# Performance work log

Hardware: AMD Instinct MI355X
Metric: run time of the kernel (lower is better)

Reference implementation:

```python
import jax, jax.numpy as jnp
import numpy as np

B, C, CE, DK, DV, H, W = 2, 64, 96, 64, 64, 96, 96
EPS = 1e-6


def setup_inputs() -> dict:
    key = jax.random.key(0)
    ks = jax.random.split(key, 8)
    s = lambda fan_in: 1.0 / np.sqrt(fan_in)
    return {
        "x": jax.random.normal(ks[0], (B, C, H, W), jnp.float32),
        "x_enc": jax.random.normal(ks[1], (B, CE, H, W), jnp.float32),
        "Wq": jax.random.uniform(ks[2], (DK, CE), jnp.float32, -s(CE), s(CE)),
        "bq": jax.random.uniform(ks[3], (DK,), jnp.float32, -s(CE), s(CE)),
        "Wk": jax.random.uniform(ks[4], (DK, CE), jnp.float32, -s(CE), s(CE)),
        "bk": jax.random.uniform(ks[5], (DK,), jnp.float32, -s(CE), s(CE)),
        "Wv": jax.random.uniform(ks[6], (DV, C), jnp.float32, -s(C), s(C)),
        "bv": jax.random.uniform(ks[7], (DV,), jnp.float32, -s(C), s(C)),
    }


def _l2norm(t):
    # F.normalize(dim=1): divide by channel-dim L2 norm, clamped at eps
    n = jnp.maximum(jnp.linalg.norm(t, axis=1, keepdims=True), EPS)
    return t / n


def reference(x, x_enc, Wq, bq, Wk, bk, Wv, bv):
    # 1x1 conv projections == pointwise channel GEMMs
    Q = jnp.einsum('oc,bchw->bohw', Wq, x_enc) + bq[None, :, None, None]
    K = jnp.einsum('oc,bchw->bohw', Wk, x_enc) + bk[None, :, None, None]
    V = jnp.einsum('oc,bchw->bohw', Wv, x) + bv[None, :, None, None]
    vshape = V.shape
    Q = _l2norm(Q.reshape(B, DK, H * W))  # [B, dk, L]
    K = _l2norm(K.reshape(B, DK, H * W))
    V = V.reshape(B, DV, H * W)           # [B, dv, L]
    # cosine-similarity attention over all spatial positions: A is [B, L, L]
    A = jax.nn.softmax(jnp.einsum('bqi,bqj->bij', Q, K), axis=-1)
    R = jnp.einsum('bij,bvj->bvi', A, V)   # [B, dv, L]
    return R.reshape(vshape)
```

## Files before the change

kernel.cpp:

```cpp
#include <hip/hip_runtime.h>

#define L_ 9216

typedef unsigned int uint;
typedef unsigned short ushort;
typedef __attribute__((ext_vector_type(8))) short short8;
typedef __attribute__((ext_vector_type(4))) float f32x4;
typedef __attribute__((ext_vector_type(16))) float f32x16;
typedef __attribute__((ext_vector_type(4))) unsigned uint4v;
typedef __attribute__((ext_vector_type(2))) unsigned uint2v;

#define MFMA32(a, b, c) __builtin_amdgcn_mfma_f32_32x32x16_bf16(a, b, c, 0, 0, 0)

#if __has_builtin(__builtin_amdgcn_exp2f)
#define EXP2(x) __builtin_amdgcn_exp2f(x)
#else
#define EXP2(x) exp2f(x)
#endif

#define GLOAD_LDS16(g, l)                                            \
  __builtin_amdgcn_global_load_lds(                                  \
      (const __attribute__((address_space(1))) unsigned int*)(g),    \
      (__attribute__((address_space(3))) unsigned int*)(l), 16, 0, 0)

union B8 {
  uint4v u;
  short8 s;
};

__device__ __forceinline__ ushort f2bf(float f) {
  uint u = __float_as_uint(f);
  return (ushort)((u + 0x7fffu + ((u >> 16) & 1u)) >> 16);
}

__device__ __forceinline__ f32x16 zero16() {
  f32x16 v;
#pragma unroll
  for (int i = 0; i < 16; i++) v[i] = 0.f;
  return v;
}

__global__ __launch_bounds__(256) void prep_kernel(
    const float* __restrict__ Wq, const float* __restrict__ Wk,
    const float* __restrict__ Wv, ushort* __restrict__ Wqb,
    ushort* __restrict__ Wkb, ushort* __restrict__ Wvb) {
  int i = blockIdx.x * 256 + threadIdx.x;
  if (i < 6144) {
    Wqb[i] = f2bf(Wq[i]);
    Wkb[i] = f2bf(Wk[i]);
  }
  if (i < 4096) Wvb[i] = f2bf(Wv[i]);
}

template <int CC, int TASK>
__device__ __forceinline__ void projm_body(
    const float* __restrict__ X,
    const ushort* __restrict__ Wb,
    const float* __restrict__ bias,
    ushort* __restrict__ dst) {
  constexpr int NKT = CC / 16;
  const int bx = blockIdx.x;
  const int b = bx / 288;
  const int p0 = (bx - b * 288) * 32;
  const int lane = threadIdx.x;
  const int ql = lane & 31;
  const int hs = lane >> 5;

  const float* Xb = X + (size_t)b * CC * L_ + p0 + ql;
  float xv[NKT * 8];
#pragma unroll
  for (int kt = 0; kt < NKT; kt++)
#pragma unroll
    for (int i = 0; i < 8; i++)
      xv[kt * 8 + i] = Xb[(size_t)(kt * 16 + hs * 8 + i) * L_];

  B8 bfr[NKT];
#pragma unroll
  for (int kt = 0; kt < NKT; kt++)
#pragma unroll
    for (int j = 0; j < 4; j++) {
      uint lo = f2bf(xv[kt * 8 + 2 * j]);
      uint hi = f2bf(xv[kt * 8 + 2 * j + 1]);
      bfr[kt].u[j] = lo | (hi << 16);
    }

  const ushort* Wr0 = Wb + (size_t)ql * CC + hs * 8;
  const ushort* Wr1 = Wb + (size_t)(32 + ql) * CC + hs * 8;

  f32x16 a0 = zero16(), a1 = zero16();
#pragma unroll
  for (int kt = 0; kt < NKT; kt++) {
    short8 w0 = *(const short8*)(Wr0 + kt * 16);
    short8 w1 = *(const short8*)(Wr1 + kt * 16);
    a0 = MFMA32(w0, bfr[kt].s, a0);
    a1 = MFMA32(w1, bfr[kt].s, a1);
  }

#pragma unroll
  for (int g = 0; g < 4; g++) {
    float4 b0 = *(const float4*)(bias + 8 * g + 4 * hs);
    float4 b1 = *(const float4*)(bias + 32 + 8 * g + 4 * hs);
    a0[4 * g + 0] += b0.x; a0[4 * g + 1] += b0.y;
    a0[4 * g + 2] += b0.z; a0[4 * g + 3] += b0.w;
    a1[4 * g + 0] += b1.x; a1[4 * g + 1] += b1.y;
    a1[4 * g + 2] += b1.z; a1[4 * g + 3] += b1.w;
  }

  if (TASK < 2) {
    float ss = 0.f;
#pragma unroll
    for (int r = 0; r < 16; r++) ss += a0[r] * a0[r] + a1[r] * a1[r];
    ss += __shfl_xor(ss, 32);
    float i0 = 1.0f / fmaxf(sqrtf(ss), 1e-6f);
    if (TASK == 0) i0 *= 1.44269504f;
    uint* d = (uint*)(dst + ((size_t)(b * L_ + p0 + ql)) * 64);
#pragma unroll
    for (int g = 0; g < 4; g++) {
      uint2v u0, u1;
      u0[0] = (uint)f2bf(a0[4 * g + 0] * i0) | ((uint)f2bf(a0[4 * g + 1] * i0) << 16);
      u0[1] = (uint)f2bf(a0[4 * g + 2] * i0) | ((uint)f2bf(a0[4 * g + 3] * i0) << 16);
      u1[0] = (uint)f2bf(a1[4 * g + 0] * i0) | ((uint)f2bf(a1[4 * g + 1] * i0) << 16);
      u1[1] = (uint)f2bf(a1[4 * g + 2] * i0) | ((uint)f2bf(a1[4 * g + 3] * i0) << 16);
      *(uint2v*)(d + 4 * g + 2 * hs) = u0;
      *(uint2v*)(d + 16 + 4 * g + 2 * hs) = u1;
    }
  } else {
#pragma unroll
    for (int r = 0; r < 16; r++) {
      int dv0 = (r & 3) + 8 * (r >> 2) + 4 * hs;
      dst[(size_t)(b * 64 + dv0) * L_ + p0 + ql] = f2bf(a0[r]);
      dst[(size_t)(b * 64 + 32 + dv0) * L_ + p0 + ql] = f2bf(a1[r]);
    }
  }
}

__global__ __launch_bounds__(64) void projm_kernel(
    const float* __restrict__ x, const float* __restrict__ x_enc,
    const ushort* __restrict__ Wqb, const float* __restrict__ bq,
    const ushort* __restrict__ Wkb, const float* __restrict__ bk,
    const ushort* __restrict__ Wvb, const float* __restrict__ bv,
    ushort* __restrict__ Qb, ushort* __restrict__ Kb,
    ushort* __restrict__ Vb) {
  const int task = blockIdx.y;
  if (task == 0)
    projm_body<96, 0>(x_enc, Wqb, bq, Qb);
  else if (task == 1)
    projm_body<96, 1>(x_enc, Wkb, bk, Kb);
  else
    projm_body<64, 2>(x, Wvb, bv, Vb);
}

__global__ __launch_bounds__(512, 4) void attn_kernel(
    const ushort* __restrict__ Qb, const ushort* __restrict__ Kb,
    const ushort* __restrict__ Vb, ushort* __restrict__ OP,
    float* __restrict__ LB, int tps) {
  __shared__ __align__(16) ushort K_l[3][64 * 64];
  __shared__ __align__(16) ushort V_l[3][64 * 64];

  const int nwg = gridDim.x;
  const int chunk = nwg >> 3;
  const int bid = blockIdx.x;
  const int logical = (bid & 7) * chunk + (bid >> 3);
  const int split = logical / 72;
  const int qidx = logical - split * 72;
  const int b = qidx / 36;
  const int q0 = (qidx - b * 36) * 256;

  const int t = threadIdx.x;
  const int lane = t & 63;
  const int w = t >> 6;
  const int ql = lane & 31;
  const int hs = lane >> 5;

  const ushort* Kg = Kb + (size_t)b * L_ * 64;
  const ushort* Vg = Vb + (size_t)b * 64 * L_;

  const int qrow = q0 + w * 32 + ql;
  const ushort* Qr = Qb + ((size_t)(b * L_ + qrow)) * 64 + hs * 8;
  short8 qf[4];
  qf[0] = *(const short8*)(Qr);
  qf[1] = *(const short8*)(Qr + 16);
  qf[2] = *(const short8*)(Qr + 32);
  qf[3] = *(const short8*)(Qr + 48);

  B8 onesu;
  onesu.u[0] = 0x3F803F80u;
  onesu.u[1] = 0x3F803F80u;
  onesu.u[2] = 0x3F803F80u;
  onesu.u[3] = 0x3F803F80u;

  f32x16 o[2];
  o[0] = zero16();
  o[1] = zero16();
  f32x16 od = zero16();

  const int rr = t >> 3, pl = t & 7;
  const int psrc = (pl ^ (rr & 7)) << 3;
  const int j0base = split * tps * 64;

#define STAGE(buf, j0)                                                       \
  {                                                                          \
    GLOAD_LDS16(Kg + (size_t)(j0)*64 + rr * 64 + psrc, &K_l[buf][w * 512]);  \
    GLOAD_LDS16(Vg + (size_t)rr * L_ + (j0) + psrc, &V_l[buf][w * 512]);     \
  }

  STAGE(0, j0base);
  STAGE(1, j0base + 64);

  int cur = 0;
  for (int tt = 0; tt < tps; tt++) {
    if (tt + 1 < tps) {
      asm volatile("s_waitcnt vmcnt(2)" ::: "memory");
    } else {
      asm volatile("s_waitcnt vmcnt(0)" ::: "memory");
    }
    __builtin_amdgcn_s_barrier();
    __builtin_amdgcn_sched_barrier(0);
    if (tt + 2 < tps) {
      int nb = cur + 2;
      if (nb >= 3) nb -= 3;
      STAGE(nb, j0base + (tt + 2) * 64);
    }
    const ushort* Kc = K_l[cur];
    const ushort* Vc = V_l[cur];

    B8 pf[4];
#pragma unroll
    for (int st = 0; st < 2; st++) {
      const int krow = st * 32 + ql;
      const int ksw = (krow & 7) << 3;
      f32x16 sa = zero16();
      __builtin_amdgcn_s_setprio(1);
#pragma unroll
      for (int m = 0; m < 4; m++) {
        short8 kf = *(const short8*)&Kc[(krow * 64 + m * 16 + hs * 8) ^ ksw];
        sa = MFMA32(kf, qf[m], sa);
      }
      __builtin_amdgcn_s_setprio(0);
      uint Wp[8];
#pragma unroll
      for (int c = 0; c < 4; c++)
#pragma unroll
        for (int rp = 0; rp < 2; rp++) {
          int i0 = 4 * c + 2 * rp;
          float p0 = EXP2(sa[i0]);
          float p1 = EXP2(sa[i0 + 1]);
          Wp[2 * c + rp] = __builtin_amdgcn_perm(
              __float_as_uint(p1), __float_as_uint(p0), 0x07060302u);
        }
#pragma unroll
      for (int u = 0; u < 2; u++) {
        auto ra = __builtin_amdgcn_permlane32_swap(Wp[4 * u + 0], Wp[4 * u + 2],
                                                   false, false);
        auto rb = __builtin_amdgcn_permlane32_swap(Wp[4 * u + 1], Wp[4 * u + 3],
                                                   false, false);
        uint4v fw;
        fw[0] = ra[0];
        fw[1] = rb[0];
        fw[2] = ra[1];
        fw[3] = rb[1];
        pf[st * 2 + u].u = fw;
      }
    }

    __builtin_amdgcn_s_setprio(1);
#pragma unroll
    for (int s = 0; s < 4; s++) od = MFMA32(onesu.s, pf[s].s, od);

#pragma unroll
    for (int dt = 0; dt < 2; dt++) {
      const int vrow = dt * 32 + ql;
      const int vsw = (vrow & 7) << 3;
#pragma unroll
      for (int s = 0; s < 4; s++) {
        short8 vf = *(const short8*)&Vc[(vrow * 64 + s * 16 + hs * 8) ^ vsw];
        o[dt] = MFMA32(vf, pf[s].s, o[dt]);
      }
    }
    __builtin_amdgcn_s_setprio(0);

    cur = (cur + 1 == 3) ? 0 : cur + 1;
  }

  if (hs == 0) LB[(size_t)split * 2 * L_ + (size_t)b * L_ + qrow] = od[0];

  ushort* Ob = OP + (size_t)split * 2 * 64 * L_;
#pragma unroll
  for (int dt = 0; dt < 2; dt++)
#pragma unroll
    for (int r = 0; r < 16; r++) {
      int dv = dt * 32 + (r & 3) + 8 * (r >> 2) + 4 * hs;
      Ob[(size_t)(b * 64 + dv) * L_ + qrow] = f2bf(o[dt][r]);
    }
}

template <int NS>
__global__ __launch_bounds__(256) void combine_kernel(
    const ushort* __restrict__ OP, const float* __restrict__ LB,
    float* __restrict__ out) {
  const size_t e = ((size_t)blockIdx.x * 256 + threadIdx.x) * 8;
  const int bdv = (int)(e / L_);
  const int b = bdv >> 6;
  const int q = (int)(e % L_);
  float os[8], ls[8];
#pragma unroll
  for (int i = 0; i < 8; i++) { os[i] = 0.f; ls[i] = 0.f; }
#pragma unroll
  for (int s = 0; s < NS; s++) {
    uint4v pv = *(const uint4v*)(OP + (size_t)s * 2 * 64 * L_ + e);
    const float* lp = LB + (size_t)s * 2 * L_ + (size_t)b * L_ + q;
    f32x4 l0 = *(const f32x4*)(lp);
    f32x4 l1 = *(const f32x4*)(lp + 4);
#pragma unroll
    for (int i = 0; i < 4; i++) {
      os[2 * i] += __uint_as_float(pv[i] << 16);
      os[2 * i + 1] += __uint_as_float(pv[i] & 0xFFFF0000u);
      ls[i] += l0[i];
      ls[4 + i] += l1[i];
    }
  }
  float r[8];
#pragma unroll
  for (int i = 0; i < 8; i++) r[i] = os[i] / ls[i];
  *(f32x4*)(out + e) = *(const f32x4*)&r[0];
  *(f32x4*)(out + e + 4) = *(const f32x4*)&r[4];
}

extern "C" void kernel_launch(void* const* d_in, const int* in_sizes, int n_in,
                              void* d_out, int out_size, void* d_ws, size_t ws_size,
                              hipStream_t stream) {
  const float* x = (const float*)d_in[0];
  const float* x_enc = (const float*)d_in[1];
  const float* Wq = (const float*)d_in[2];
  const float* bq = (const float*)d_in[3];
  const float* Wk = (const float*)d_in[4];
  const float* bk = (const float*)d_in[5];
  const float* Wv = (const float*)d_in[6];
  const float* bv = (const float*)d_in[7];
  float* out = (float*)d_out;

  ushort* Qb = (ushort*)d_ws;
  ushort* Kb = Qb + (size_t)2 * L_ * 64;
  ushort* Vb = Kb + (size_t)2 * L_ * 64;
  ushort* Wqb = Vb + (size_t)2 * L_ * 64;
  ushort* Wkb = Wqb + 6144;
  ushort* Wvb = Wkb + 6144;
  const size_t qkv_bytes = (size_t)3 * 2 * L_ * 64 * 2 + 2 * (6144 + 6144 + 4096);
  const size_t per_split = (size_t)2 * 64 * L_ * 2 + (size_t)2 * L_ * 4;

  int SPLIT = 8;
  while (SPLIT > 1 && qkv_bytes + (size_t)SPLIT * per_split > ws_size) SPLIT >>= 1;

  ushort* OP = (ushort*)((char*)d_ws + qkv_bytes);
  float* LB = (float*)(OP + (size_t)SPLIT * 2 * 64 * L_);

  prep_kernel<<<24, 256, 0, stream>>>(Wq, Wk, Wv, Wqb, Wkb, Wvb);
  projm_kernel<<<dim3(576, 3), 64, 0, stream>>>(x, x_enc, Wqb, bq, Wkb, bk,
                                                Wvb, bv, Qb, Kb, Vb);
  attn_kernel<<<72 * SPLIT, 512, 0, stream>>>(Qb, Kb, Vb, OP, LB, 144 / SPLIT);
  const int cgrid = (2 * 64 * L_ / 8) / 256;
  if (SPLIT == 8)
    combine_kernel<8><<<cgrid, 256, 0, stream>>>(OP, LB, out);
  else if (SPLIT == 4)
    combine_kernel<4><<<cgrid, 256, 0, stream>>>(OP, LB, out);
  else if (SPLIT == 2)
    combine_kernel<2><<<cgrid, 256, 0, stream>>>(OP, LB, out);
  else
    combine_kernel<1><<<cgrid, 256, 0, stream>>>(OP, LB, out);
}
```

Baseline: 86.49 us.

## Unroll attention loop by ring depth, double the KV split, raise occupancy

The attention main loop is unrolled by three to match the triple-buffered LDS ring. K and V now share one LDS array, so per-lane fragment addresses are precomputed once and buffer offsets become compile-time constants. This removes the per-iteration buffer-index arithmetic and swizzle recomputation. The KV split factor rises from 8 to 16, giving twice as many workgroups with half the KV tiles each, and the launch-bounds occupancy hint goes from 4 to 6. In exchange, the combine kernel has to merge twice as many bf16 partials, the workspace grows, and the higher occupancy hint may force register spills, while LDS size still caps how many blocks fit per CU.

```diff
diff --git a/kernel.cpp b/kernel.cpp
--- a/kernel.cpp
+++ b/kernel.cpp
@@ -150,12 +150,11 @@
     projm_body<64, 2>(x, Wvb, bv, Vb);
 }
 
-__global__ __launch_bounds__(512, 4) void attn_kernel(
+__global__ __launch_bounds__(512, 6) void attn_kernel(
     const ushort* __restrict__ Qb, const ushort* __restrict__ Kb,
     const ushort* __restrict__ Vb, ushort* __restrict__ OP,
     float* __restrict__ LB, int tps) {
-  __shared__ __align__(16) ushort K_l[3][64 * 64];
-  __shared__ __align__(16) ushort V_l[3][64 * 64];
+  __shared__ __align__(16) ushort KV_l[3][2][4096];
 
   const int nwg = gridDim.x;
   const int chunk = nwg >> 3;
@@ -194,92 +193,97 @@
   o[1] = zero16();
   f32x16 od = zero16();
 
+  const int ksw = (ql & 7) << 3;
+  const char* lds0 = (const char*)&KV_l[0][0][0];
+  int arf[4];
+#pragma unroll
+  for (int m = 0; m < 4; m++)
+    arf[m] = (ql * 64 + ((m * 16 + hs * 8) ^ ksw)) * 2;
+
   const int rr = t >> 3, pl = t & 7;
   const int psrc = (pl ^ (rr & 7)) << 3;
   const int j0base = split * tps * 64;
 
-#define STAGE(buf, j0)                                                       \
-  {                                                                          \
-    GLOAD_LDS16(Kg + (size_t)(j0)*64 + rr * 64 + psrc, &K_l[buf][w * 512]);  \
-    GLOAD_LDS16(Vg + (size_t)rr * L_ + (j0) + psrc, &V_l[buf][w * 512]);     \
+#define STAGE(buf, j0)                                                     \
+  {                                                                        \
+    GLOAD_LDS16(Kg + (size_t)(j0)*64 + rr * 64 + psrc,                     \
+                &KV_l[buf][0][w * 512]);                                   \
+    GLOAD_LDS16(Vg + (size_t)rr * L_ + (j0) + psrc,                        \
+                &KV_l[buf][1][w * 512]);                                   \
   }
 
   STAGE(0, j0base);
   STAGE(1, j0base + 64);
 
-  int cur = 0;
-  for (int tt = 0; tt < tps; tt++) {
-    if (tt + 1 < tps) {
-      asm volatile("s_waitcnt vmcnt(2)" ::: "memory");
-    } else {
-      asm volatile("s_waitcnt vmcnt(0)" ::: "memory");
-    }
-    __builtin_amdgcn_s_barrier();
-    __builtin_amdgcn_sched_barrier(0);
-    if (tt + 2 < tps) {
-      int nb = cur + 2;
-      if (nb >= 3) nb -= 3;
-      STAGE(nb, j0base + (tt + 2) * 64);
-    }
-    const ushort* Kc = K_l[cur];
-    const ushort* Vc = V_l[cur];
-
-    B8 pf[4];
-#pragma unroll
-    for (int st = 0; st < 2; st++) {
-      const int krow = st * 32 + ql;
-      const int ksw = (krow & 7) << 3;
-      f32x16 sa = zero16();
+  for (int t3 = 0; t3 < tps; t3 += 3) {
+#pragma unroll
+    for (int ib = 0; ib < 3; ib++) {
+      const int tt = t3 + ib;
+      if (tt + 1 < tps) {
+        asm volatile("s_waitcnt vmcnt(2)" ::: "memory");
+      } else {
+        asm volatile("s_waitcnt vmcnt(0)" ::: "memory");
+      }
+      __builtin_amdgcn_s_barrier();
+      __builtin_amdgcn_sched_barrier(0);
+      if (tt + 2 < tps) {
+        STAGE((ib + 2) % 3, j0base + (tt + 2) * 64);
+      }
+
+      B8 pf[4];
+#pragma unroll
+      for (int st = 0; st < 2; st++) {
+        f32x16 sa = zero16();
+        __builtin_amdgcn_s_setprio(1);
+#pragma unroll
+        for (int m = 0; m < 4; m++) {
+          short8 kf = *(const short8*)(lds0 + arf[m] + ib * 16384 + st * 4096);
+          sa = MFMA32(kf, qf[m], sa);
+        }
+        __builtin_amdgcn_s_setprio(0);
+        uint Wp[8];
+#pragma unroll
+        for (int c = 0; c < 4; c++)
+#pragma unroll
+          for (int rp = 0; rp < 2; rp++) {
+            int i0 = 4 * c + 2 * rp;
+            float p0 = EXP2(sa[i0]);
+            float p1 = EXP2(sa[i0 + 1]);
+            Wp[2 * c + rp] = __builtin_amdgcn_perm(
+                __float_as_uint(p1), __float_as_uint(p0), 0x07060302u);
+          }
+#pragma unroll
+        for (int u = 0; u < 2; u++) {
+          auto ra = __builtin_amdgcn_permlane32_swap(Wp[4 * u + 0],
+                                                     Wp[4 * u + 2], false,
+                                                     false);
+          auto rb = __builtin_amdgcn_permlane32_swap(Wp[4 * u + 1],
+                                                     Wp[4 * u + 3], false,
+                                                     false);
+          uint4v fw;
+          fw[0] = ra[0];
+          fw[1] = rb[0];
+          fw[2] = ra[1];
+          fw[3] = rb[1];
+          pf[st * 2 + u].u = fw;
+        }
+      }
+
       __builtin_amdgcn_s_setprio(1);
 #pragma unroll
-      for (int m = 0; m < 4; m++) {
-        short8 kf = *(const short8*)&Kc[(krow * 64 + m * 16 + hs * 8) ^ ksw];
-        sa = MFMA32(kf, qf[m], sa);
+      for (int s = 0; s < 4; s++) od = MFMA32(onesu.s, pf[s].s, od);
+
+#pragma unroll
+      for (int dt = 0; dt < 2; dt++) {
+#pragma unroll
+        for (int s = 0; s < 4; s++) {
+          short8 vf = *(const short8*)(lds0 + arf[s] + ib * 16384 + 8192 +
+                                       dt * 4096);
+          o[dt] = MFMA32(vf, pf[s].s, o[dt]);
+        }
       }
       __builtin_amdgcn_s_setprio(0);
-      uint Wp[8];
-#pragma unroll
-      for (int c = 0; c < 4; c++)
-#pragma unroll
-        for (int rp = 0; rp < 2; rp++) {
-          int i0 = 4 * c + 2 * rp;
-          float p0 = EXP2(sa[i0]);
-          float p1 = EXP2(sa[i0 + 1]);
-          Wp[2 * c + rp] = __builtin_amdgcn_perm(
-              __float_as_uint(p1), __float_as_uint(p0), 0x07060302u);
-        }
-#pragma unroll
-      for (int u = 0; u < 2; u++) {
-        auto ra = __builtin_amdgcn_permlane32_swap(Wp[4 * u + 0], Wp[4 * u + 2],
-                                                   false, false);
-        auto rb = __builtin_amdgcn_permlane32_swap(Wp[4 * u + 1], Wp[4 * u + 3],
-                                                   false, false);
-        uint4v fw;
-        fw[0] = ra[0];
-        fw[1] = rb[0];
-        fw[2] = ra[1];
-        fw[3] = rb[1];
-        pf[st * 2 + u].u = fw;
-      }
-    }
-
-    __builtin_amdgcn_s_setprio(1);
-#pragma unroll
-    for (int s = 0; s < 4; s++) od = MFMA32(onesu.s, pf[s].s, od);
-
-#pragma unroll
-    for (int dt = 0; dt < 2; dt++) {
-      const int vrow = dt * 32 + ql;
-      const int vsw = (vrow & 7) << 3;
-#pragma unroll
-      for (int s = 0; s < 4; s++) {
-        short8 vf = *(const short8*)&Vc[(vrow * 64 + s * 16 + hs * 8) ^ vsw];
-        o[dt] = MFMA32(vf, pf[s].s, o[dt]);
-      }
-    }
-    __builtin_amdgcn_s_setprio(0);
-
-    cur = (cur + 1 == 3) ? 0 : cur + 1;
+    }
   }
 
   if (hs == 0) LB[(size_t)split * 2 * L_ + (size_t)b * L_ + qrow] = od[0];
@@ -348,7 +352,7 @@
   const size_t qkv_bytes = (size_t)3 * 2 * L_ * 64 * 2 + 2 * (6144 + 6144 + 4096);
   const size_t per_split = (size_t)2 * 64 * L_ * 2 + (size_t)2 * L_ * 4;
 
-  int SPLIT = 8;
+  int SPLIT = 16;
   while (SPLIT > 1 && qkv_bytes + (size_t)SPLIT * per_split > ws_size) SPLIT >>= 1;
 
   ushort* OP = (ushort*)((char*)d_ws + qkv_bytes);
@@ -359,7 +363,9 @@
                                                 Wvb, bv, Qb, Kb, Vb);
   attn_kernel<<<72 * SPLIT, 512, 0, stream>>>(Qb, Kb, Vb, OP, LB, 144 / SPLIT);
   const int cgrid = (2 * 64 * L_ / 8) / 256;
-  if (SPLIT == 8)
+  if (SPLIT == 16)
+    combine_kernel<16><<<cgrid, 256, 0, stream>>>(OP, LB, out);
+  else if (SPLIT == 8)
     combine_kernel<8><<<cgrid, 256, 0, stream>>>(OP, LB, out);
   else if (SPLIT == 4)
     combine_kernel<4><<<cgrid, 256, 0, stream>>>(OP, LB, out);
```

After: 209.0 us. 2.42x slower.

## Load K/V fragments directly from global memory, dropping LDS staging

Applied to the files above, without the earlier changes.

Replaces the triple-buffered LDS staging of K and V tiles (global_load_lds plus barriers) with per-lane direct global loads of the MFMA fragments into registers. Workgroups shrink from 512 to 256 threads, covering 128 queries each, and the grid doubles to compensate. This removes LDS traffic and block-wide barriers. In exchange, each wave re-reads K/V from global/L2 with no sharing across waves and no prefetch pipeline, so load latency is exposed unless occupancy hides it. V reads are strided across rows of length L.

```diff
diff --git a/kernel.cpp b/kernel.cpp
--- a/kernel.cpp
+++ b/kernel.cpp
@@ -17,11 +17,6 @@
 #else
 #define EXP2(x) exp2f(x)
 #endif
-
-#define GLOAD_LDS16(g, l)                                            \
-  __builtin_amdgcn_global_load_lds(                                  \
-      (const __attribute__((address_space(1))) unsigned int*)(g),    \
-      (__attribute__((address_space(3))) unsigned int*)(l), 16, 0, 0)
 
 union B8 {
   uint4v u;
@@ -150,21 +145,18 @@
     projm_body<64, 2>(x, Wvb, bv, Vb);
 }
 
-__global__ __launch_bounds__(512, 4) void attn_kernel(
+__global__ __launch_bounds__(256, 2) void attn_kernel(
     const ushort* __restrict__ Qb, const ushort* __restrict__ Kb,
     const ushort* __restrict__ Vb, ushort* __restrict__ OP,
     float* __restrict__ LB, int tps) {
-  __shared__ __align__(16) ushort K_l[3][64 * 64];
-  __shared__ __align__(16) ushort V_l[3][64 * 64];
-
   const int nwg = gridDim.x;
   const int chunk = nwg >> 3;
   const int bid = blockIdx.x;
   const int logical = (bid & 7) * chunk + (bid >> 3);
-  const int split = logical / 72;
-  const int qidx = logical - split * 72;
-  const int b = qidx / 36;
-  const int q0 = (qidx - b * 36) * 256;
+  const int split = logical / 144;
+  const int qidx = logical - split * 144;
+  const int b = qidx / 72;
+  const int q0 = (qidx - b * 72) * 128;
 
   const int t = threadIdx.x;
   const int lane = t & 63;
@@ -194,48 +186,33 @@
   o[1] = zero16();
   f32x16 od = zero16();
 
-  const int rr = t >> 3, pl = t & 7;
-  const int psrc = (pl ^ (rr & 7)) << 3;
   const int j0base = split * tps * 64;
-
-#define STAGE(buf, j0)                                                       \
-  {                                                                          \
-    GLOAD_LDS16(Kg + (size_t)(j0)*64 + rr * 64 + psrc, &K_l[buf][w * 512]);  \
-    GLOAD_LDS16(Vg + (size_t)rr * L_ + (j0) + psrc, &V_l[buf][w * 512]);     \
-  }
-
-  STAGE(0, j0base);
-  STAGE(1, j0base + 64);
-
-  int cur = 0;
+  const ushort* Kp0 = Kg + ((size_t)(j0base + ql)) * 64 + hs * 8;
+  const ushort* Vp0 = Vg + (size_t)ql * L_ + j0base + hs * 8;
+
   for (int tt = 0; tt < tps; tt++) {
-    if (tt + 1 < tps) {
-      asm volatile("s_waitcnt vmcnt(2)" ::: "memory");
-    } else {
-      asm volatile("s_waitcnt vmcnt(0)" ::: "memory");
-    }
-    __builtin_amdgcn_s_barrier();
-    __builtin_amdgcn_sched_barrier(0);
-    if (tt + 2 < tps) {
-      int nb = cur + 2;
-      if (nb >= 3) nb -= 3;
-      STAGE(nb, j0base + (tt + 2) * 64);
-    }
-    const ushort* Kc = K_l[cur];
-    const ushort* Vc = V_l[cur];
+    short8 kf[2][4];
+#pragma unroll
+    for (int st = 0; st < 2; st++)
+#pragma unroll
+      for (int m = 0; m < 4; m++)
+        kf[st][m] =
+            *(const short8*)(Kp0 + (size_t)(tt * 64 + st * 32) * 64 + m * 16);
+    short8 vf[2][4];
+#pragma unroll
+    for (int dt = 0; dt < 2; dt++)
+#pragma unroll
+      for (int s = 0; s < 4; s++)
+        vf[dt][s] = *(const short8*)(Vp0 + (size_t)dt * 32 * L_ + tt * 64 +
+                                     s * 16);
 
     B8 pf[4];
 #pragma unroll
     for (int st = 0; st < 2; st++) {
-      const int krow = st * 32 + ql;
-      const int ksw = (krow & 7) << 3;
       f32x16 sa = zero16();
       __builtin_amdgcn_s_setprio(1);
 #pragma unroll
-      for (int m = 0; m < 4; m++) {
-        short8 kf = *(const short8*)&Kc[(krow * 64 + m * 16 + hs * 8) ^ ksw];
-        sa = MFMA32(kf, qf[m], sa);
-      }
+      for (int m = 0; m < 4; m++) sa = MFMA32(kf[st][m], qf[m], sa);
       __builtin_amdgcn_s_setprio(0);
       uint Wp[8];
 #pragma unroll
@@ -268,18 +245,10 @@
     for (int s = 0; s < 4; s++) od = MFMA32(onesu.s, pf[s].s, od);
 
 #pragma unroll
-    for (int dt = 0; dt < 2; dt++) {
-      const int vrow = dt * 32 + ql;
-      const int vsw = (vrow & 7) << 3;
-#pragma unroll
-      for (int s = 0; s < 4; s++) {
-        short8 vf = *(const short8*)&Vc[(vrow * 64 + s * 16 + hs * 8) ^ vsw];
-        o[dt] = MFMA32(vf, pf[s].s, o[dt]);
-      }
-    }
+    for (int dt = 0; dt < 2; dt++)
+#pragma unroll
+      for (int s = 0; s < 4; s++) o[dt] = MFMA32(vf[dt][s], pf[s].s, o[dt]);
     __builtin_amdgcn_s_setprio(0);
-
-    cur = (cur + 1 == 3) ? 0 : cur + 1;
   }
 
   if (hs == 0) LB[(size_t)split * 2 * L_ + (size_t)b * L_ + qrow] = od[0];
@@ -357,7 +326,7 @@
   prep_kernel<<<24, 256, 0, stream>>>(Wq, Wk, Wv, Wqb, Wkb, Wvb);
   projm_kernel<<<dim3(576, 3), 64, 0, stream>>>(x, x_enc, Wqb, bq, Wkb, bk,
                                                 Wvb, bv, Qb, Kb, Vb);
-  attn_kernel<<<72 * SPLIT, 512, 0, stream>>>(Qb, Kb, Vb, OP, LB, 144 / SPLIT);
+  attn_kernel<<<144 * SPLIT, 256, 0, stream>>>(Qb, Kb, Vb, OP, LB, 144 / SPLIT);
   const int cgrid = (2 * 64 * L_ / 8) / 256;
   if (SPLIT == 8)
     combine_kernel<8><<<cgrid, 256, 0, stream>>>(OP, LB, out);
```

After: 188.1 us. +117.5%, slower.
